# Kernel tuning notes

Measured on AMD Instinct MI355X. Metric: run time of the kernel, lower is better.

The kernel has to match this reference:

```python
import jax, jax.numpy as jnp
import numpy as np

B, N, D, H = 2, 2048, 1024, 16
DH = D // H
DF = 4 * D
SCALE = D ** (-0.5)  # standard_scale=False -> dim**-0.5
EPS = 1e-5


def _ln(x, w, b):
    mu = jnp.mean(x, axis=-1, keepdims=True)
    var = jnp.mean(jnp.square(x - mu), axis=-1, keepdims=True)
    return (x - mu) * jax.lax.rsqrt(var + EPS) * w + b


def setup_inputs() -> dict:
    key = jax.random.key(0)
    ks = jax.random.split(key, 12)
    s = lambda fan_in: (1.0 / np.sqrt(fan_in))
    return {
        "x": jax.random.normal(ks[0], (B, N, D), jnp.float32),
        "gamma": jax.random.uniform(ks[1], (B, H), jnp.float32),
        "dist_matrix": jax.random.uniform(ks[2], (N, N), jnp.float32),
        "ln1_w": jnp.ones((D,), jnp.float32),
        "ln1_b": jnp.zeros((D,), jnp.float32),
        "qkv_w": jax.random.normal(ks[3], (D, 3 * D), jnp.float32) * s(D),
        "qkv_b": jnp.zeros((3 * D,), jnp.float32),
        "proj_w": jax.random.normal(ks[4], (D, D), jnp.float32) * s(D),
        "proj_b": jnp.zeros((D,), jnp.float32),
        "ln2_w": jnp.ones((D,), jnp.float32),
        "ln2_b": jnp.zeros((D,), jnp.float32),
        "mlp_w1": jax.random.normal(ks[5], (D, DF), jnp.float32) * s(D),
        "mlp_b1": jnp.zeros((DF,), jnp.float32),
        "mlp_w2": jax.random.normal(ks[6], (DF, D), jnp.float32) * s(DF),
        "mlp_b2": jnp.zeros((D,), jnp.float32),
    }


def reference(x, gamma, dist_matrix, ln1_w, ln1_b, qkv_w, qkv_b, proj_w, proj_b,
              ln2_w, ln2_b, mlp_w1, mlp_b1, mlp_w2, mlp_b2):
    # --- ZoomAttention on norm1(x) ---
    h = _ln(x, ln1_w, ln1_b)                                   # [B,N,D]
    qkv = h @ qkv_w + qkv_b                                    # [B,N,3D]
    qkv = qkv.reshape(B, N, 3, H, DH).transpose(2, 0, 3, 1, 4)  # [3,B,H,N,DH]
    q, k, v = qkv[0], qkv[1], qkv[2]
    scores = jnp.einsum("bhnd,bhmd->bhnm", q, k) * SCALE       # [B,H,N,N]
    scores = scores - gamma[:, :, None, None] * dist_matrix[None, None]
    attn = jax.nn.softmax(scores, axis=-1)
    out = jnp.einsum("bhnm,bhmd->bhnd", attn, v)               # [B,H,N,DH]
    out = out.transpose(0, 2, 1, 3).reshape(B, N, D)
    x = x + (out @ proj_w + proj_b)
    # --- MLP (exact GELU, torch default) ---
    h2 = _ln(x, ln2_w, ln2_b)
    h2 = jax.nn.gelu(h2 @ mlp_w1 + mlp_b1, approximate=False) @ mlp_w2 + mlp_b2
    return x + h2
```

## Files before the change

### kernel.cpp

```cpp
#include <hip/hip_runtime.h>
#include <hip/hip_bf16.h>


#define SCALE_ 0.03125f
#define EPS_   1e-5f
#define LOG2E_ 1.4426950408889634f
#define SC2_   (SCALE_ * LOG2E_)

typedef unsigned short u16;
typedef __attribute__((ext_vector_type(8))) short short8;
typedef __attribute__((ext_vector_type(4))) float f32x4;
typedef __attribute__((ext_vector_type(4))) unsigned short u16x4;

__device__ inline float b2f(u16 u){ unsigned x = ((unsigned)u) << 16; float f; __builtin_memcpy(&f, &x, 4); return f; }
__device__ inline u16 f2b(float f){ __hip_bfloat16 h = __float2bfloat16(f); u16 u; __builtin_memcpy(&u, &h, 2); return u; }

__device__ inline void glds16(const u16* g, u16* l) {
    __builtin_amdgcn_global_load_lds(
        (const __attribute__((address_space(1))) void*)g,
        (__attribute__((address_space(3))) void*)l, 16, 0, 0);
}

__device__ inline unsigned cvtpk(float a, float b) {
    unsigned r;
    asm("v_cvt_pk_bf16_f32 %0, %1, %2" : "=v"(r) : "v"(a), "v"(b));
    return r;
}

__global__ __launch_bounds__(256) void transpose_cast(const float* __restrict__ src,
                                                      u16* __restrict__ dst, int K, int N) {
    __shared__ float t[32][33];
    int nb = blockIdx.x * 32, kb = blockIdx.y * 32;
    int tx = threadIdx.x & 31, ty = threadIdx.x >> 5;
    for (int i = 0; i < 4; i++) {
        int r = ty + i * 8;
        t[r][tx] = src[(size_t)(kb + r) * N + nb + tx];
    }
    __syncthreads();
    for (int i = 0; i < 4; i++) {
        int r = ty + i * 8;
        dst[(size_t)(nb + r) * K + kb + tx] = f2b(t[tx][r]);
    }
}

__global__ __launch_bounds__(256) void cast_scale_bf16(const float* __restrict__ src,
                                                       u16* __restrict__ dst, int n4, float scale) {
    int i = blockIdx.x * 256 + threadIdx.x;
    if (i < n4) {
        float4 v = ((const float4*)src)[i];
        u16x4 o;
        o[0] = f2b(v.x * scale); o[1] = f2b(v.y * scale);
        o[2] = f2b(v.z * scale); o[3] = f2b(v.w * scale);
        ((u16x4*)dst)[i] = o;
    }
}

__global__ __launch_bounds__(256) void ln_bf16(const float* __restrict__ x,
                                               const float* __restrict__ w,
                                               const float* __restrict__ b,
                                               u16* __restrict__ out) {
    int row = blockIdx.x, t = threadIdx.x;
    float4 v = ((const float4*)(x + (size_t)row * 1024))[t];
    float s1 = v.x + v.y + v.z + v.w;
    float s2 = v.x * v.x + v.y * v.y + v.z * v.z + v.w * v.w;
    for (int o = 32; o > 0; o >>= 1) { s1 += __shfl_xor(s1, o); s2 += __shfl_xor(s2, o); }
    __shared__ float a1[4], a2[4];
    if ((t & 63) == 0) { a1[t >> 6] = s1; a2[t >> 6] = s2; }
    __syncthreads();
    s1 = a1[0] + a1[1] + a1[2] + a1[3];
    s2 = a2[0] + a2[1] + a2[2] + a2[3];
    float mu = s1 * (1.0f / 1024.0f);
    float var = s2 * (1.0f / 1024.0f) - mu * mu;
    float rs = rsqrtf(var + EPS_);
    float4 wv = ((const float4*)w)[t];
    float4 bv = ((const float4*)b)[t];
    u16x4 o;
    o[0] = f2b((v.x - mu) * rs * wv.x + bv.x);
    o[1] = f2b((v.y - mu) * rs * wv.y + bv.y);
    o[2] = f2b((v.z - mu) * rs * wv.z + bv.z);
    o[3] = f2b((v.w - mu) * rs * wv.w + bv.w);
    ((u16x4*)(out + (size_t)row * 1024))[t] = o;
}

template <int MODE>
__global__ __launch_bounds__(512) void gemm256_8ph(
    const u16* __restrict__ A, const u16* __restrict__ Bt,
    const float* __restrict__ bias, int K,
    u16* __restrict__ outb,
    u16* __restrict__ qp, u16* __restrict__ kp, u16* __restrict__ vtp) {
    __shared__ u16 LS[4][2][256 * 32];
    int tid = threadIdx.x;
    int w = tid >> 6, lane = tid & 63, g = lane >> 4, ln = lane & 15;
    int wr = w >> 2, wc = w & 3;
    int gx = gridDim.x;
    int nwg = gx * gridDim.y;
    int lin = blockIdx.y * gx + blockIdx.x;
    int swz = (lin & 7) * (nwg >> 3) + (lin >> 3);
    int bx = swz % gx, by = swz / gx;
    int br = by * 256, bc = bx * 256;
    int jx = (((lane & 3) ^ ((lane >> 3) & 3)) << 3);
    const u16* Ast = A + (size_t)(br + w * 32 + (lane >> 2)) * K + jx;
    const u16* Bst = Bt + (size_t)(bc + w * 32 + (lane >> 2)) * K + jx;
    size_t r16 = (size_t)16 * K;
    const int ldsW = (w * 32) * 32;
    f32x4 acc[8][4] = {};
    int NT = K >> 5;
    int slotr = ((g ^ ((ln >> 1) & 3)) << 3);
    for (int kt = 0; kt < 3; ++kt) {
        glds16(Ast + (size_t)kt * 32, &LS[kt][0][ldsW]);
        glds16(Ast + (size_t)kt * 32 + r16, &LS[kt][0][ldsW + 512]);
        glds16(Bst + (size_t)kt * 32, &LS[kt][1][ldsW]);
        glds16(Bst + (size_t)kt * 32 + r16, &LS[kt][1][ldsW + 512]);
    }
    asm volatile("s_waitcnt vmcnt(8)" ::: "memory");
    __builtin_amdgcn_s_barrier();
    short8 aa[4], bb[4];
    for (int kt = 0; kt < NT; ++kt) {
        const u16* bufA = &LS[kt & 3][0][0];
        const u16* bufB = &LS[kt & 3][1][0];
        int s3 = kt + 3;
        #pragma unroll
        for (int m = 0; m < 4; ++m)
            aa[m] = *(const short8*)&bufA[(wr * 128 + m * 16 + ln) * 32 + slotr];
        #pragma unroll
        for (int n = 0; n < 4; ++n)
            bb[n] = *(const short8*)&bufB[(wc * 64 + n * 16 + ln) * 32 + slotr];
        if (s3 < NT) {
            u16* d = &LS[s3 & 3][0][ldsW];
            glds16(Ast + (size_t)s3 * 32, d);
            glds16(Ast + (size_t)s3 * 32 + r16, d + 512);
        }
        __builtin_amdgcn_s_barrier();
        asm volatile("s_waitcnt lgkmcnt(0)" ::: "memory");
        __builtin_amdgcn_sched_barrier(0);
        __builtin_amdgcn_s_setprio(1);
        #pragma unroll
        for (int m = 0; m < 4; ++m)
            #pragma unroll
            for (int n = 0; n < 4; ++n)
                acc[m][n] = __builtin_amdgcn_mfma_f32_16x16x32_bf16(aa[m], bb[n], acc[m][n], 0, 0, 0);
        __builtin_amdgcn_s_setprio(0);
        __builtin_amdgcn_sched_barrier(0);
        __builtin_amdgcn_s_barrier();
        #pragma unroll
        for (int m = 0; m < 4; ++m)
            aa[m] = *(const short8*)&bufA[(wr * 128 + 64 + m * 16 + ln) * 32 + slotr];
        if (s3 < NT) {
            u16* d = &LS[s3 & 3][1][ldsW];
            glds16(Bst + (size_t)s3 * 32, d);
            glds16(Bst + (size_t)s3 * 32 + r16, d + 512);
        }
        if (kt + 3 < NT)      asm volatile("s_waitcnt vmcnt(8)" ::: "memory");
        else if (kt + 2 < NT) asm volatile("s_waitcnt vmcnt(4)" ::: "memory");
        else if (kt + 1 < NT) asm volatile("s_waitcnt vmcnt(0)" ::: "memory");
        __builtin_amdgcn_s_barrier();
        asm volatile("s_waitcnt lgkmcnt(0)" ::: "memory");
        __builtin_amdgcn_sched_barrier(0);
        __builtin_amdgcn_s_setprio(1);
        #pragma unroll
        for (int m = 0; m < 4; ++m)
            #pragma unroll
            for (int n = 0; n < 4; ++n)
                acc[4 + m][n] = __builtin_amdgcn_mfma_f32_16x16x32_bf16(aa[m], bb[n], acc[4 + m][n], 0, 0, 0);
        __builtin_amdgcn_s_setprio(0);
        __builtin_amdgcn_sched_barrier(0);
        __builtin_amdgcn_s_barrier();
    }
    #pragma unroll
    for (int m = 0; m < 8; ++m) {
        int row0 = br + wr * 128 + m * 16 + g * 4;
        #pragma unroll
        for (int n = 0; n < 4; ++n) {
            int col = bc + wc * 64 + n * 16 + ln;
            float bv = bias[col];
            if constexpr (MODE == 0) {
                int which = col >> 10, cc = col & 1023, hh = cc >> 6, dh = cc & 63;
                int bb2 = row0 >> 11, nn0 = row0 & 2047;
                size_t bh = (size_t)(bb2 * 16 + hh);
                if (which == 0) {
                    for (int r = 0; r < 4; r++)
                        qp[((bh * 2048 + nn0 + r) << 6) + dh] = f2b((acc[m][n][r] + bv) * SC2_);
                } else if (which == 1) {
                    for (int r = 0; r < 4; r++)
                        kp[((bh * 2048 + nn0 + r) << 6) + dh] = f2b(acc[m][n][r] + bv);
                } else {
                    u16x4 o;
                    for (int r = 0; r < 4; r++) o[r] = f2b(acc[m][n][r] + bv);
                    *(u16x4*)&vtp[((bh * 64 + dh) << 11) + nn0] = o;
                }
            } else {
                for (int r = 0; r < 4; r++) {
                    float v = acc[m][n][r] + bv;
                    float gl = 0.5f * v * (1.0f + erff(v * 0.7071067811865476f));
                    outb[(size_t)(row0 + r) * 4096 + col] = f2b(gl);
                }
            }
        }
    }
}

template <int MODE, int BN>
__global__ __launch_bounds__(256) void gemm_bf16(
    const u16* __restrict__ A, const u16* __restrict__ Bt,
    const float* __restrict__ bias, int M, int N, int K,
    const float* __restrict__ res, float* __restrict__ outf) {
    constexpr int NN = BN / 32;
    __shared__ u16 As[128 * 64];
    __shared__ u16 Bs[BN * 64];
    int br = blockIdx.y * 128, bc = blockIdx.x * BN;
    int tid = threadIdx.x;
    int w = tid >> 6, lane = tid & 63, g = lane >> 4, ln = lane & 15;
    int wr = (w >> 1) * 64, wc = (w & 1) * (BN / 2);
    f32x4 acc[4][NN] = {};
    int sgcol = (((lane & 7) ^ (lane >> 3)) << 3);
    int arow = w * 32 + (lane >> 3);
    int brow = w * (BN / 4) + (lane >> 3);
    const u16* Ap = A + (size_t)(br + arow) * K + sgcol;
    const u16* Bp = Bt + (size_t)(bc + brow) * K + sgcol;
    u16* lA = &As[(w * 32) * 64];
    u16* lB = &Bs[(w * (BN / 4)) * 64];
    size_t rstep = (size_t)8 * K;
    for (int kt = 0; kt < K; kt += 64) {
        __syncthreads();
        #pragma unroll
        for (int i = 0; i < 4; i++) glds16(Ap + kt + i * rstep, lA + i * 512);
        #pragma unroll
        for (int i = 0; i < BN / 32; i++) glds16(Bp + kt + i * rstep, lB + i * 512);
        __syncthreads();
        #pragma unroll
        for (int kk = 0; kk < 2; kk++) {
            int so = (((kk << 2) + g) ^ (ln & 7)) << 3;
            short8 af[4], bfr[NN];
            #pragma unroll
            for (int m = 0; m < 4; m++)  af[m]  = *(const short8*)&As[(wr + m * 16 + ln) * 64 + so];
            #pragma unroll
            for (int n = 0; n < NN; n++) bfr[n] = *(const short8*)&Bs[(wc + n * 16 + ln) * 64 + so];
            #pragma unroll
            for (int m = 0; m < 4; m++)
                #pragma unroll
                for (int n = 0; n < NN; n++)
                    acc[m][n] = __builtin_amdgcn_mfma_f32_16x16x32_bf16(af[m], bfr[n], acc[m][n], 0, 0, 0);
        }
    }
    #pragma unroll
    for (int m = 0; m < 4; m++) {
        int row0 = br + wr + m * 16 + g * 4;
        #pragma unroll
        for (int n = 0; n < NN; n++) {
            int col = bc + wc + n * 16 + ln;
            float bv = bias[col];
            if constexpr (MODE == 1) {
                for (int r = 0; r < 4; r++) {
                    size_t idx = (size_t)(row0 + r) * 1024 + col;
                    outf[idx] = res[idx] + acc[m][n][r] + bv;
                }
            } else {
                for (int r = 0; r < 4; r++) {
                    size_t idx = (size_t)(row0 + r) * 1024 + col;
                    outf[idx] = outf[idx] + acc[m][n][r] + bv;
                }
            }
        }
    }
}

__global__ __launch_bounds__(512) void attn_fwd(
    const u16* __restrict__ qg, const u16* __restrict__ kg, const u16* __restrict__ vtg,
    const u16* __restrict__ distb, const float* __restrict__ gamma, u16* __restrict__ ao) {
    __shared__ u16 Ks[2][64 * 64];
    __shared__ u16 Vs[2][64 * 64];
    __shared__ u16 Ps[8][16 * 64];
    int qt = blockIdx.x, bh = blockIdx.y;
    int b = bh >> 4, h = bh & 15;
    int tid = threadIdx.x, w = tid >> 6, lane = tid & 63, g = lane >> 4, ln = lane & 15;
    float gam = gamma[bh];
    int qglob = qt * 128 + w * 16 + ln;
    const u16* qrow = qg + ((size_t)bh * 2048 + qglob) * 64;
    short8 qf0 = *(const short8*)(qrow + g * 8);
    short8 qf1 = *(const short8*)(qrow + 32 + g * 8);
    const u16* dbase = distb + (size_t)qglob * 2048 + g * 4;
    float m2 = -3.0e38f, lsum = 0.0f;
    f32x4 acco[4] = {};
    int srow = tid >> 3, seg = tid & 7;
    int ss = ((seg ^ (srow & 7)) << 3);
    const u16* kgp = kg + ((size_t)bh * 2048 + srow) * 64 + seg * 8;
    const u16* vgp = vtg + ((size_t)bh * 64 + srow) * 2048 + seg * 8;
    {
        short8 a0 = *(const short8*)(kgp);
        short8 c0 = *(const short8*)(vgp);
        *(short8*)&Ks[0][srow * 64 + ss] = a0;
        *(short8*)&Vs[0][srow * 64 + ss] = c0;
    }
    u16x4 dcv[4];
    #pragma unroll
    for (int nb = 0; nb < 4; nb++) dcv[nb] = *(const u16x4*)(dbase + nb * 16);
    __syncthreads();
    int cur = 0;
    int so0 = (g ^ (ln & 7)) << 3, so1 = ((4 + g) ^ (ln & 7)) << 3;
    for (int kt = 0; kt < 32; kt++) {
        short8 kr0, vr0;
        u16x4 dnx[4];
        if (kt < 31) {
            kr0 = *(const short8*)(kgp + (kt + 1) * 4096);
            vr0 = *(const short8*)(vgp + (kt + 1) * 64);
            #pragma unroll
            for (int nb = 0; nb < 4; nb++)
                dnx[nb] = *(const u16x4*)(dbase + (kt + 1) * 64 + nb * 16);
        }
        f32x4 sa[4] = {};
        __builtin_amdgcn_s_setprio(1);
        #pragma unroll
        for (int nb = 0; nb < 4; nb++) {
            short8 kf0 = *(const short8*)&Ks[cur][(nb * 16 + ln) * 64 + so0];
            short8 kf1 = *(const short8*)&Ks[cur][(nb * 16 + ln) * 64 + so1];
            sa[nb] = __builtin_amdgcn_mfma_f32_16x16x32_bf16(kf0, qf0, sa[nb], 0, 0, 0);
            sa[nb] = __builtin_amdgcn_mfma_f32_16x16x32_bf16(kf1, qf1, sa[nb], 0, 0, 0);
        }
        __builtin_amdgcn_s_setprio(0);
        float sv[4][4], pm = -3.0e38f;
        #pragma unroll
        for (int nb = 0; nb < 4; nb++) {
            #pragma unroll
            for (int r = 0; r < 4; r++)
                sv[nb][r] = sa[nb][r] - gam * b2f(dcv[nb][r]);
            pm = fmaxf(pm, fmaxf(fmaxf(sv[nb][0], sv[nb][1]), fmaxf(sv[nb][2], sv[nb][3])));
        }
        pm = fmaxf(pm, __shfl_xor(pm, 16));
        pm = fmaxf(pm, __shfl_xor(pm, 32));
        if (!__all(pm - m2 <= 8.0f)) {
            float nm = fmaxf(m2, pm);
            float al = __builtin_exp2f(m2 - nm);
            m2 = nm;
            lsum *= al;
            #pragma unroll
            for (int db = 0; db < 4; db++) acco[db] *= al;
        }
        float ps = 0.0f;
        #pragma unroll
        for (int nb = 0; nb < 4; nb++) {
            float e0 = __builtin_exp2f(sv[nb][0] - m2);
            float e1 = __builtin_exp2f(sv[nb][1] - m2);
            float e2 = __builtin_exp2f(sv[nb][2] - m2);
            float e3 = __builtin_exp2f(sv[nb][3] - m2);
            ps += (e0 + e1) + (e2 + e3);
            union { unsigned u[2]; u16x4 v; } pk;
            pk.u[0] = cvtpk(e0, e1);
            pk.u[1] = cvtpk(e2, e3);
            int off = nb * 16 + g * 4;
            *(u16x4*)&Ps[w][ln * 64 + (((off >> 3) ^ (ln & 7)) << 3) + (off & 7)] = pk.v;
        }
        ps += __shfl_xor(ps, 16);
        ps += __shfl_xor(ps, 32);
        lsum += ps;
        short8 pf0 = *(const short8*)&Ps[w][ln * 64 + so0];
        short8 pf1 = *(const short8*)&Ps[w][ln * 64 + so1];
        __builtin_amdgcn_s_setprio(1);
        #pragma unroll
        for (int db = 0; db < 4; db++) {
            short8 vf0 = *(const short8*)&Vs[cur][(db * 16 + ln) * 64 + so0];
            short8 vf1 = *(const short8*)&Vs[cur][(db * 16 + ln) * 64 + so1];
            acco[db] = __builtin_amdgcn_mfma_f32_16x16x32_bf16(vf0, pf0, acco[db], 0, 0, 0);
            acco[db] = __builtin_amdgcn_mfma_f32_16x16x32_bf16(vf1, pf1, acco[db], 0, 0, 0);
        }
        __builtin_amdgcn_s_setprio(0);
        if (kt < 31) {
            int nx = cur ^ 1;
            *(short8*)&Ks[nx][srow * 64 + ss] = kr0;
            *(short8*)&Vs[nx][srow * 64 + ss] = vr0;
            #pragma unroll
            for (int nb = 0; nb < 4; nb++) dcv[nb] = dnx[nb];
            __syncthreads();
            cur = nx;
        }
    }
    float inv = 1.0f / lsum;
    u16* aop = ao + (size_t)(b * 2048 + qglob) * 1024 + h * 64 + g * 4;
    #pragma unroll
    for (int db = 0; db < 4; db++) {
        u16x4 o;
        #pragma unroll
        for (int r = 0; r < 4; r++) o[r] = f2b(acco[db][r] * inv);
        *(u16x4*)(aop + db * 16) = o;
    }
}

extern "C" void kernel_launch(void* const* d_in, const int* in_sizes, int n_in,
                              void* d_out, int out_size, void* d_ws, size_t ws_size,
                              hipStream_t stream) {
    const float* x     = (const float*)d_in[0];
    const float* gamma = (const float*)d_in[1];
    const float* dist  = (const float*)d_in[2];
    const float* ln1w  = (const float*)d_in[3];
    const float* ln1b  = (const float*)d_in[4];
    const float* qkvw  = (const float*)d_in[5];
    const float* qkvb  = (const float*)d_in[6];
    const float* projw = (const float*)d_in[7];
    const float* projb = (const float*)d_in[8];
    const float* ln2w  = (const float*)d_in[9];
    const float* ln2b  = (const float*)d_in[10];
    const float* w1    = (const float*)d_in[11];
    const float* b1    = (const float*)d_in[12];
    const float* w2    = (const float*)d_in[13];
    const float* b2    = (const float*)d_in[14];
    float* out = (float*)d_out;
    char* ws = (char*)d_ws;
    u16* wqkvT  = (u16*)(ws + 0);
    u16* wprojT = (u16*)(ws + 6291456);
    u16* w1T    = (u16*)(ws + 8388608);
    u16* w2T    = (u16*)(ws + 16777216);
    u16* distb  = (u16*)(ws + 25165824);
    u16* hb     = (u16*)(ws + 33554432);
    u16* qb     = (u16*)(ws + 41943040);
    u16* kb     = (u16*)(ws + 50331648);
    u16* vtb    = (u16*)(ws + 58720256);
    u16* aob    = (u16*)(ws + 67108864);
    u16* gb     = hb;
    u16* h2b    = aob;

    dim3 blk(256);
    transpose_cast<<<dim3(3072 / 32, 1024 / 32), blk, 0, stream>>>(qkvw, wqkvT, 1024, 3072);
    transpose_cast<<<dim3(1024 / 32, 1024 / 32), blk, 0, stream>>>(projw, wprojT, 1024, 1024);
    transpose_cast<<<dim3(4096 / 32, 1024 / 32), blk, 0, stream>>>(w1, w1T, 1024, 4096);
    transpose_cast<<<dim3(1024 / 32, 4096 / 32), blk, 0, stream>>>(w2, w2T, 4096, 1024);
    cast_scale_bf16<<<4096, blk, 0, stream>>>(dist, distb, 2048 * 2048 / 4, LOG2E_);
    ln_bf16<<<4096, blk, 0, stream>>>(x, ln1w, ln1b, hb);
    gemm256_8ph<0><<<dim3(12, 16), dim3(512), 0, stream>>>(hb, wqkvT, qkvb, 1024,
                                                           nullptr, qb, kb, vtb);
    attn_fwd<<<dim3(16, 32), dim3(512), 0, stream>>>(qb, kb, vtb, distb, gamma, aob);
    gemm_bf16<1, 64><<<dim3(16, 32), blk, 0, stream>>>(aob, wprojT, projb, 4096, 1024, 1024,
                                                       x, out);
    ln_bf16<<<4096, blk, 0, stream>>>(out, ln2w, ln2b, h2b);
    gemm256_8ph<2><<<dim3(16, 16), dim3(512), 0, stream>>>(h2b, w1T, b1, 1024,
                                                           gb, nullptr, nullptr, nullptr);
    gemm_bf16<3, 64><<<dim3(16, 32), blk, 0, stream>>>(gb, w2T, b2, 4096, 1024, 4096,
                                                       nullptr, out);
}
```

Measured before the change: 282.9 us.

## Split-K MLP down-projection on 256-tile kernel with atomics; read fp32 dist directly

The second MLP GEMM (K=4096) moves from the 128xBN gemm_bf16 kernel to the 256x256 8-phase kernel. K is split four ways across blockIdx.z and partial results are accumulated into the residual output with atomicAdd, and only the first slice adds the bias. Separately, the dist-matrix bf16 cast kernel is removed and attention reads fp32 dist directly, with log2e folded into gamma. This trades one extra kernel pass for twice the dist bytes inside attention, and fp32 atomics make the summation order nondeterministic.

```diff
diff --git a/kernel.cpp b/kernel.cpp
--- a/kernel.cpp
+++ b/kernel.cpp
@@ -40,18 +40,6 @@
     for (int i = 0; i < 4; i++) {
         int r = ty + i * 8;
         dst[(size_t)(nb + r) * K + kb + tx] = f2b(t[tx][r]);
-    }
-}
-
-__global__ __launch_bounds__(256) void cast_scale_bf16(const float* __restrict__ src,
-                                                       u16* __restrict__ dst, int n4, float scale) {
-    int i = blockIdx.x * 256 + threadIdx.x;
-    if (i < n4) {
-        float4 v = ((const float4*)src)[i];
-        u16x4 o;
-        o[0] = f2b(v.x * scale); o[1] = f2b(v.y * scale);
-        o[2] = f2b(v.z * scale); o[3] = f2b(v.w * scale);
-        ((u16x4*)dst)[i] = o;
     }
 }
 
@@ -85,8 +73,8 @@
 template <int MODE>
 __global__ __launch_bounds__(512) void gemm256_8ph(
     const u16* __restrict__ A, const u16* __restrict__ Bt,
-    const float* __restrict__ bias, int K,
-    u16* __restrict__ outb,
+    const float* __restrict__ bias, int K, int ksl,
+    u16* __restrict__ outb, float* __restrict__ outf,
     u16* __restrict__ qp, u16* __restrict__ kp, u16* __restrict__ vtp) {
     __shared__ u16 LS[4][2][256 * 32];
     int tid = threadIdx.x;
@@ -98,13 +86,14 @@
     int swz = (lin & 7) * (nwg >> 3) + (lin >> 3);
     int bx = swz % gx, by = swz / gx;
     int br = by * 256, bc = bx * 256;
+    int k0 = blockIdx.z * ksl;
     int jx = (((lane & 3) ^ ((lane >> 3) & 3)) << 3);
-    const u16* Ast = A + (size_t)(br + w * 32 + (lane >> 2)) * K + jx;
-    const u16* Bst = Bt + (size_t)(bc + w * 32 + (lane >> 2)) * K + jx;
+    const u16* Ast = A + (size_t)(br + w * 32 + (lane >> 2)) * K + k0 + jx;
+    const u16* Bst = Bt + (size_t)(bc + w * 32 + (lane >> 2)) * K + k0 + jx;
     size_t r16 = (size_t)16 * K;
     const int ldsW = (w * 32) * 32;
     f32x4 acc[8][4] = {};
-    int NT = K >> 5;
+    int NT = ksl >> 5;
     int slotr = ((g ^ ((ln >> 1) & 3)) << 3);
     for (int kt = 0; kt < 3; ++kt) {
         glds16(Ast + (size_t)kt * 32, &LS[kt][0][ldsW]);
@@ -172,8 +161,8 @@
         #pragma unroll
         for (int n = 0; n < 4; ++n) {
             int col = bc + wc * 64 + n * 16 + ln;
-            float bv = bias[col];
             if constexpr (MODE == 0) {
+                float bv = bias[col];
                 int which = col >> 10, cc = col & 1023, hh = cc >> 6, dh = cc & 63;
                 int bb2 = row0 >> 11, nn0 = row0 & 2047;
                 size_t bh = (size_t)(bb2 * 16 + hh);
@@ -188,12 +177,17 @@
                     for (int r = 0; r < 4; r++) o[r] = f2b(acc[m][n][r] + bv);
                     *(u16x4*)&vtp[((bh * 64 + dh) << 11) + nn0] = o;
                 }
-            } else {
+            } else if constexpr (MODE == 2) {
+                float bv = bias[col];
                 for (int r = 0; r < 4; r++) {
                     float v = acc[m][n][r] + bv;
                     float gl = 0.5f * v * (1.0f + erff(v * 0.7071067811865476f));
                     outb[(size_t)(row0 + r) * 4096 + col] = f2b(gl);
                 }
+            } else {
+                float bv = (k0 == 0) ? bias[col] : 0.0f;
+                for (int r = 0; r < 4; r++)
+                    atomicAdd(&outf[(size_t)(row0 + r) * 1024 + col], acc[m][n][r] + bv);
             }
         }
     }
@@ -249,16 +243,9 @@
         for (int n = 0; n < NN; n++) {
             int col = bc + wc + n * 16 + ln;
             float bv = bias[col];
-            if constexpr (MODE == 1) {
-                for (int r = 0; r < 4; r++) {
-                    size_t idx = (size_t)(row0 + r) * 1024 + col;
-                    outf[idx] = res[idx] + acc[m][n][r] + bv;
-                }
-            } else {
-                for (int r = 0; r < 4; r++) {
-                    size_t idx = (size_t)(row0 + r) * 1024 + col;
-                    outf[idx] = outf[idx] + acc[m][n][r] + bv;
-                }
+            for (int r = 0; r < 4; r++) {
+                size_t idx = (size_t)(row0 + r) * 1024 + col;
+                outf[idx] = res[idx] + acc[m][n][r] + bv;
             }
         }
     }
@@ -266,19 +253,19 @@
 
 __global__ __launch_bounds__(512) void attn_fwd(
     const u16* __restrict__ qg, const u16* __restrict__ kg, const u16* __restrict__ vtg,
-    const u16* __restrict__ distb, const float* __restrict__ gamma, u16* __restrict__ ao) {
+    const float* __restrict__ dist, const float* __restrict__ gamma, u16* __restrict__ ao) {
     __shared__ u16 Ks[2][64 * 64];
     __shared__ u16 Vs[2][64 * 64];
     __shared__ u16 Ps[8][16 * 64];
     int qt = blockIdx.x, bh = blockIdx.y;
     int b = bh >> 4, h = bh & 15;
     int tid = threadIdx.x, w = tid >> 6, lane = tid & 63, g = lane >> 4, ln = lane & 15;
-    float gam = gamma[bh];
+    float gam = gamma[bh] * LOG2E_;
     int qglob = qt * 128 + w * 16 + ln;
     const u16* qrow = qg + ((size_t)bh * 2048 + qglob) * 64;
     short8 qf0 = *(const short8*)(qrow + g * 8);
     short8 qf1 = *(const short8*)(qrow + 32 + g * 8);
-    const u16* dbase = distb + (size_t)qglob * 2048 + g * 4;
+    const float* dbase = dist + (size_t)qglob * 2048 + g * 4;
     float m2 = -3.0e38f, lsum = 0.0f;
     f32x4 acco[4] = {};
     int srow = tid >> 3, seg = tid & 7;
@@ -291,21 +278,21 @@
         *(short8*)&Ks[0][srow * 64 + ss] = a0;
         *(short8*)&Vs[0][srow * 64 + ss] = c0;
     }
-    u16x4 dcv[4];
+    f32x4 dcv[4];
     #pragma unroll
-    for (int nb = 0; nb < 4; nb++) dcv[nb] = *(const u16x4*)(dbase + nb * 16);
+    for (int nb = 0; nb < 4; nb++) dcv[nb] = *(const f32x4*)(dbase + nb * 16);
     __syncthreads();
     int cur = 0;
     int so0 = (g ^ (ln & 7)) << 3, so1 = ((4 + g) ^ (ln & 7)) << 3;
     for (int kt = 0; kt < 32; kt++) {
         short8 kr0, vr0;
-        u16x4 dnx[4];
+        f32x4 dnx[4];
         if (kt < 31) {
             kr0 = *(const short8*)(kgp + (kt + 1) * 4096);
             vr0 = *(const short8*)(vgp + (kt + 1) * 64);
             #pragma unroll
             for (int nb = 0; nb < 4; nb++)
-                dnx[nb] = *(const u16x4*)(dbase + (kt + 1) * 64 + nb * 16);
+                dnx[nb] = *(const f32x4*)(dbase + (kt + 1) * 64 + nb * 16);
         }
         f32x4 sa[4] = {};
         __builtin_amdgcn_s_setprio(1);
@@ -322,7 +309,7 @@
         for (int nb = 0; nb < 4; nb++) {
             #pragma unroll
             for (int r = 0; r < 4; r++)
-                sv[nb][r] = sa[nb][r] - gam * b2f(dcv[nb][r]);
+                sv[nb][r] = sa[nb][r] - gam * dcv[nb][r];
             pm = fmaxf(pm, fmaxf(fmaxf(sv[nb][0], sv[nb][1]), fmaxf(sv[nb][2], sv[nb][3])));
         }
         pm = fmaxf(pm, __shfl_xor(pm, 16));
@@ -408,7 +395,6 @@
     u16* wprojT = (u16*)(ws + 6291456);
     u16* w1T    = (u16*)(ws + 8388608);
     u16* w2T    = (u16*)(ws + 16777216);
-    u16* distb  = (u16*)(ws + 25165824);
     u16* hb     = (u16*)(ws + 33554432);
     u16* qb     = (u16*)(ws + 41943040);
     u16* kb     = (u16*)(ws + 50331648);
@@ -422,16 +408,15 @@
     transpose_cast<<<dim3(1024 / 32, 1024 / 32), blk, 0, stream>>>(projw, wprojT, 1024, 1024);
     transpose_cast<<<dim3(4096 / 32, 1024 / 32), blk, 0, stream>>>(w1, w1T, 1024, 4096);
     transpose_cast<<<dim3(1024 / 32, 4096 / 32), blk, 0, stream>>>(w2, w2T, 4096, 1024);
-    cast_scale_bf16<<<4096, blk, 0, stream>>>(dist, distb, 2048 * 2048 / 4, LOG2E_);
     ln_bf16<<<4096, blk, 0, stream>>>(x, ln1w, ln1b, hb);
-    gemm256_8ph<0><<<dim3(12, 16), dim3(512), 0, stream>>>(hb, wqkvT, qkvb, 1024,
-                                                           nullptr, qb, kb, vtb);
-    attn_fwd<<<dim3(16, 32), dim3(512), 0, stream>>>(qb, kb, vtb, distb, gamma, aob);
+    gemm256_8ph<0><<<dim3(12, 16), dim3(512), 0, stream>>>(hb, wqkvT, qkvb, 1024, 1024,
+                                                           nullptr, nullptr, qb, kb, vtb);
+    attn_fwd<<<dim3(16, 32), dim3(512), 0, stream>>>(qb, kb, vtb, dist, gamma, aob);
     gemm_bf16<1, 64><<<dim3(16, 32), blk, 0, stream>>>(aob, wprojT, projb, 4096, 1024, 1024,
                                                        x, out);
     ln_bf16<<<4096, blk, 0, stream>>>(out, ln2w, ln2b, h2b);
-    gemm256_8ph<2><<<dim3(16, 16), dim3(512), 0, stream>>>(h2b, w1T, b1, 1024,
-                                                           gb, nullptr, nullptr, nullptr);
-    gemm_bf16<3, 64><<<dim3(16, 32), blk, 0, stream>>>(gb, w2T, b2, 4096, 1024, 4096,
-                                                       nullptr, out);
-}
+    gemm256_8ph<2><<<dim3(16, 16), dim3(512), 0, stream>>>(h2b, w1T, b1, 1024, 1024,
+                                                           gb, nullptr, nullptr, nullptr, nullptr);
+    gemm256_8ph<3><<<dim3(4, 16, 4), dim3(512), 0, stream>>>(gb, w2T, b2, 4096, 1024,
+                                                             nullptr, out, nullptr, nullptr, nullptr);
+}
```

New measurement: 292.9 us. 3.6% more time.
